# Kernel optimization log

Hardware: AMD Instinct MI355X
Metric: run time of the kernel (lower is better)

The kernel has to match this reference:

```python
import jax, jax.numpy as jnp
import numpy as np

NUM_EXPERTS = 8
D_MODEL = 2048
D_FF = 4096
TOP_K = 2
NUM_TOKENS = 4096


def setup_inputs() -> dict:
    key = jax.random.key(0)
    k1, k2, k3, k4, k5, k6 = jax.random.split(key, 6)
    hidden_states = jax.random.normal(k1, (NUM_TOKENS, D_MODEL), dtype=jnp.float32)
    top_k_index = jax.random.randint(k2, (NUM_TOKENS, TOP_K), 0, NUM_EXPERTS)
    raw = jax.random.uniform(k3, (NUM_TOKENS, TOP_K), dtype=jnp.float32)
    top_k_weights = raw / jnp.sum(raw, axis=-1, keepdims=True)  # normalized router weights
    scale = 0.02
    Wg = jax.random.normal(k4, (NUM_EXPERTS, D_MODEL, D_FF), dtype=jnp.float32) * scale
    Wu = jax.random.normal(k5, (NUM_EXPERTS, D_MODEL, D_FF), dtype=jnp.float32) * scale
    Wd = jax.random.normal(k6, (NUM_EXPERTS, D_FF, D_MODEL), dtype=jnp.float32) * scale
    return {
        "hidden_states": hidden_states,
        "top_k_index": top_k_index,
        "top_k_weights": top_k_weights,
        "Wg": Wg,
        "Wu": Wu,
        "Wd": Wd,
    }


def reference(hidden_states, top_k_index, top_k_weights, Wg, Wu, Wd):
    T, D = hidden_states.shape
    E = Wg.shape[0]
    # Combine weights: [T, E], summing duplicate expert hits exactly as the
    # original loop's repeated index_add_ would.
    combine = jnp.zeros((T, E), dtype=top_k_weights.dtype)
    combine = combine.at[jnp.arange(T)[:, None], top_k_index].add(top_k_weights)
    # Dense all-experts SwiGLU (same math per token/expert as the gather loop)
    gate = jnp.einsum("td,edf->tef", hidden_states, Wg)   # [T, E, F]
    up = jnp.einsum("td,edf->tef", hidden_states, Wu)     # [T, E, F]
    h = jax.nn.silu(gate) * up                              # [T, E, F]
    expert_out = jnp.einsum("tef,efd->ted", h, Wd)          # [T, E, D]
    # Weighted scatter-combine
    final = jnp.einsum("ted,te->td", expert_out, combine)   # [T, D]
    return final
```

## Files before the change

### kernel.cpp

```cpp
#include <hip/hip_runtime.h>
#include <hip/hip_bf16.h>

#define NTOK 4096
#define DM   2048
#define DF   4096
#define NEXP 8
#define NPAD 10240
#define NPTILE 40

typedef __attribute__((ext_vector_type(4))) float f32x4;
typedef __attribute__((ext_vector_type(8))) short s16x8;
typedef __attribute__((ext_vector_type(2))) int   i32x2;

__device__ __forceinline__ unsigned short f2bf(float f) {
  union { float f; unsigned u; } x; x.f = f;
  unsigned r = x.u + 0x7fffu + ((x.u >> 16) & 1u);
  return (unsigned short)(r >> 16);
}
__device__ __forceinline__ unsigned pack2(float lo, float hi) {
  __hip_bfloat162 h2 = __float22bfloat162_rn(make_float2(lo, hi));
  return *reinterpret_cast<unsigned*>(&h2);
}
__device__ __forceinline__ int swz(int row, int ks) {
  return row * 32 + ((ks ^ ((row >> 1) & 3)) << 3);
}
__device__ __forceinline__ void g2l16(const void* g, void* l) {
  __builtin_amdgcn_global_load_lds(
      (const __attribute__((address_space(1))) void*)g,
      (__attribute__((address_space(3))) void*)l, 16, 0, 0);
}

#define BARRIER() asm volatile("s_barrier" ::: "memory")
#define WAITV(n)  asm volatile("s_waitcnt vmcnt(" #n ")" ::: "memory")

__global__ void k_zero_out(float* out) {
  int gid = blockIdx.x * 256 + threadIdx.x;
  *(f32x4*)(out + (size_t)gid * 4) = f32x4{0.f, 0.f, 0.f, 0.f};
}

__global__ void k_init(int* tokrow, int* counts, int* cursor) {
  int i = blockIdx.x * 256 + threadIdx.x;
  if (i < NPAD) tokrow[i] = 0;
  if (i < NEXP) { counts[i] = 0; cursor[i] = 0; }
}

__global__ void k_count(const int* __restrict__ idx, int* counts) {
  int t = blockIdx.x * 256 + threadIdx.x;
  if (t >= NTOK) return;
  int e0 = idx[2 * t], e1 = idx[2 * t + 1];
  atomicAdd(&counts[e0], 1);
  if (e1 != e0) atomicAdd(&counts[e1], 1);
}

__global__ void k_scan(const int* __restrict__ counts, int* poff) {
  if (threadIdx.x == 0) {
    int s = 0;
    for (int e = 0; e < NEXP; e++) {
      poff[e] = s;
      s += ((counts[e] + 255) & ~255);
    }
  }
}

__global__ void k_fill(const int* __restrict__ idx, const float* __restrict__ wts,
                       const int* __restrict__ poff, int* cursor,
                       int* tokrow, float* wrow) {
  int t = blockIdx.x * 256 + threadIdx.x;
  if (t >= NTOK) return;
  int e0 = idx[2 * t], e1 = idx[2 * t + 1];
  float w0 = wts[2 * t], w1 = wts[2 * t + 1];
  if (e0 == e1) {
    int g = poff[e0] + atomicAdd(&cursor[e0], 1);
    tokrow[g] = t; wrow[g] = w0 + w1;
  } else {
    int g0 = poff[e0] + atomicAdd(&cursor[e0], 1);
    tokrow[g0] = t; wrow[g0] = w0;
    int g1 = poff[e1] + atomicAdd(&cursor[e1], 1);
    tokrow[g1] = t; wrow[g1] = w1;
  }
}

__global__ void k_convX(const float* __restrict__ X, const int* __restrict__ tokrow,
                        short* __restrict__ Xg) {
  const int kt = blockIdx.x, tile = blockIdx.y, tid = threadIdx.x;
  const int part = tid & 7;
  short* dst = Xg + (size_t)(tile * 64 + kt) * 8192;
  #pragma unroll
  for (int it = 0; it < 8; it++) {
    int row = it * 32 + (tid >> 3);
    int tok = tokrow[tile * 256 + row];
    f32x4 v = *(const f32x4*)(X + (size_t)tok * DM + kt * 32 + part * 4);
    i32x2 p;
    p[0] = (int)pack2(v[0], v[1]);
    p[1] = (int)pack2(v[2], v[3]);
    int idx = row * 32 + (((part >> 1) ^ ((row >> 1) & 3)) << 3) + (part & 1) * 4;
    *(i32x2*)&dst[idx] = p;
  }
}

__global__ void k_convW(const float* __restrict__ W, short* __restrict__ dst,
                        int N, int K) {
  const int nt = blockIdx.x, kt = blockIdx.y, e = blockIdx.z;
  const int t = threadIdx.x;
  const int kg = t >> 5, nb = t & 31;
  const float* src = W + (size_t)e * K * N + (size_t)(kt * 32 + kg * 4) * N
                     + nt * 128 + nb * 4;
  f32x4 b0 = *(const f32x4*)(src);
  f32x4 b1 = *(const f32x4*)(src + N);
  f32x4 b2 = *(const f32x4*)(src + 2 * (size_t)N);
  f32x4 b3 = *(const f32x4*)(src + 3 * (size_t)N);
  short* img = dst + ((size_t)(e * (N / 128) + nt) * (K / 32) + kt) * 4096;
  const int c0 = kg >> 1, klo = (kg & 1) * 4;
  #pragma unroll
  for (int j = 0; j < 4; j++) {
    int nl = nb * 4 + j;
    i32x2 v;
    v[0] = (int)pack2(b0[j], b1[j]);
    v[1] = (int)pack2(b2[j], b3[j]);
    *(i32x2*)&img[nl * 32 + ((c0 ^ ((nl >> 1) & 3)) << 3) + klo] = v;
  }
}

__global__ __launch_bounds__(512, 2) void gemm1_kernel(
    const short* __restrict__ Xg, const short* __restrict__ Wgt,
    const short* __restrict__ Wut, const int* __restrict__ counts,
    const int* __restrict__ poff, unsigned short* __restrict__ Hs) {
  const int e = blockIdx.z;
  const int cnt = counts[e];
  const int m0 = blockIdx.y * 256;
  if (m0 >= cnt) return;
  const int nt = blockIdx.x, n0 = nt * 128;
  const int tileIdx = (poff[e] >> 8) + blockIdx.y;

  __shared__ __attribute__((aligned(16))) short As[4][8192];
  __shared__ __attribute__((aligned(16))) short Bs[4][2][4096];

  const int tid = threadIdx.x, wave = tid >> 6, lane = tid & 63;
  const int wm = wave >> 1, wn = wave & 1;
  const int lr = lane & 15, ks = lane >> 4;

  const short* aSrc = Xg + (size_t)tileIdx * 64 * 8192 + wave * 1024 + lane * 8;
  const short* gSrc = Wgt + (size_t)(e * 32 + nt) * 64 * 4096 + wave * 512 + lane * 8;
  const short* uSrc = Wut + (size_t)(e * 32 + nt) * 64 * 4096 + wave * 512 + lane * 8;

  f32x4 accg[4][4], accu[4][4];
  #pragma unroll
  for (int i = 0; i < 4; i++)
    #pragma unroll
    for (int j = 0; j < 4; j++) {
      accg[i][j] = f32x4{0.f, 0.f, 0.f, 0.f};
      accu[i][j] = f32x4{0.f, 0.f, 0.f, 0.f};
    }

  auto stage = [&](int s, int kt) {
    g2l16(aSrc + (size_t)kt * 8192,       &As[s][wave * 1024]);
    g2l16(aSrc + (size_t)kt * 8192 + 512, &As[s][wave * 1024 + 512]);
    g2l16(gSrc + (size_t)kt * 4096,       &Bs[s][0][wave * 512]);
    g2l16(uSrc + (size_t)kt * 4096,       &Bs[s][1][wave * 512]);
  };

  const int nK = DM / 32;
  stage(0, 0); stage(1, 1); stage(2, 2);
  asm volatile("s_waitcnt vmcnt(8) lgkmcnt(0)" ::: "memory");
  BARRIER();

  for (int kt = 0; kt < nK; ++kt) {
    const int s = kt & 3;
    if (kt + 3 < nK) stage((kt + 3) & 3, kt + 3);
    s16x8 af[4], bg[4], bu[4];
    #pragma unroll
    for (int mi = 0; mi < 4; mi++)
      af[mi] = *(const s16x8*)&As[s][swz(wm * 64 + mi * 16 + lr, ks)];
    #pragma unroll
    for (int ni = 0; ni < 4; ni++) {
      bg[ni] = *(const s16x8*)&Bs[s][0][swz(wn * 64 + ni * 16 + lr, ks)];
      bu[ni] = *(const s16x8*)&Bs[s][1][swz(wn * 64 + ni * 16 + lr, ks)];
    }
    __builtin_amdgcn_s_setprio(1);
    #pragma unroll
    for (int mi = 0; mi < 4; mi++)
      #pragma unroll
      for (int ni = 0; ni < 4; ni++) {
        accg[mi][ni] = __builtin_amdgcn_mfma_f32_16x16x32_bf16(af[mi], bg[ni], accg[mi][ni], 0, 0, 0);
        accu[mi][ni] = __builtin_amdgcn_mfma_f32_16x16x32_bf16(af[mi], bu[ni], accu[mi][ni], 0, 0, 0);
      }
    __builtin_amdgcn_s_setprio(0);
    if (kt + 1 < nK) {
      if (kt + 3 < nK)      { WAITV(8); }
      else if (kt + 2 < nK) { WAITV(4); }
      else                  { WAITV(0); }
      BARRIER();
    }
  }

  const size_t tb = (size_t)tileIdx * 128 * 8192;
  #pragma unroll
  for (int mi = 0; mi < 4; mi++) {
    #pragma unroll
    for (int r = 0; r < 4; r++) {
      int row = wm * 64 + mi * 16 + ks * 4 + r;
      if (m0 + row < cnt) {
        #pragma unroll
        for (int ni = 0; ni < 4; ni++) {
          int col = n0 + wn * 64 + ni * 16 + lr;
          float g = accg[mi][ni][r], u = accu[mi][ni][r];
          float sv = g / (1.f + __expf(-g));
          int ktH = col >> 5, kl = col & 31;
          Hs[tb + (size_t)ktH * 8192 + row * 32 +
             (((kl >> 3) ^ ((row >> 1) & 3)) << 3) + (kl & 7)] = f2bf(sv * u);
        }
      }
    }
  }
}

__global__ __launch_bounds__(256, 2) void gemm2_kernel(
    const unsigned short* __restrict__ Hs, const short* __restrict__ Wdt,
    const int* __restrict__ counts, const int* __restrict__ poff,
    const int* __restrict__ tokrow, const float* __restrict__ wrow,
    float* __restrict__ out) {
  const int e = blockIdx.z;
  const int cnt = counts[e];
  const int m0 = blockIdx.y * 128;
  if (m0 >= cnt) return;
  const int nt = blockIdx.x, n0 = nt * 256;
  const int tileIdx = (poff[e] >> 8) + (m0 >> 8);
  const int half = (m0 >> 7) & 1;
  const int roff = poff[e];

  __shared__ __attribute__((aligned(16))) short As[3][4096];
  __shared__ __attribute__((aligned(16))) short Bs[3][2][4096];

  const int tid = threadIdx.x, wave = tid >> 6, lane = tid & 63;
  const int wm = wave >> 1, wn = wave & 1;
  const int lr = lane & 15, ks = lane >> 4;

  const unsigned short* aSrc = Hs + (size_t)tileIdx * 128 * 8192 + half * 4096
                               + wave * 1024 + lane * 8;
  const short* b0Src = Wdt + (size_t)(e * 16 + 2 * nt) * 128 * 4096
                       + wave * 1024 + lane * 8;
  const short* b1Src = Wdt + (size_t)(e * 16 + 2 * nt + 1) * 128 * 4096
                       + wave * 1024 + lane * 8;

  f32x4 acc0[4][4], acc1[4][4];
  #pragma unroll
  for (int i = 0; i < 4; i++)
    #pragma unroll
    for (int j = 0; j < 4; j++) {
      acc0[i][j] = f32x4{0.f, 0.f, 0.f, 0.f};
      acc1[i][j] = f32x4{0.f, 0.f, 0.f, 0.f};
    }

  auto stage = [&](int s, int kt) {
    g2l16(aSrc + (size_t)kt * 8192,        &As[s][wave * 1024]);
    g2l16(aSrc + (size_t)kt * 8192 + 512,  &As[s][wave * 1024 + 512]);
    g2l16(b0Src + (size_t)kt * 4096,       &Bs[s][0][wave * 1024]);
    g2l16(b0Src + (size_t)kt * 4096 + 512, &Bs[s][0][wave * 1024 + 512]);
    g2l16(b1Src + (size_t)kt * 4096,       &Bs[s][1][wave * 1024]);
    g2l16(b1Src + (size_t)kt * 4096 + 512, &Bs[s][1][wave * 1024 + 512]);
  };

  const int nK = DF / 32;
  stage(0, 0); stage(1, 1);
  WAITV(6);
  BARRIER();

  for (int kt = 0; kt < nK; ++kt) {
    const int s = kt % 3;
    if (kt + 2 < nK) stage((kt + 2) % 3, kt + 2);
    s16x8 af[4], b0f[4], b1f[4];
    #pragma unroll
    for (int mi = 0; mi < 4; mi++)
      af[mi] = *(const s16x8*)&As[s][swz(wm * 64 + mi * 16 + lr, ks)];
    #pragma unroll
    for (int ni = 0; ni < 4; ni++) {
      b0f[ni] = *(const s16x8*)&Bs[s][0][swz(wn * 64 + ni * 16 + lr, ks)];
      b1f[ni] = *(const s16x8*)&Bs[s][1][swz(wn * 64 + ni * 16 + lr, ks)];
    }
    __builtin_amdgcn_s_setprio(1);
    #pragma unroll
    for (int mi = 0; mi < 4; mi++)
      #pragma unroll
      for (int ni = 0; ni < 4; ni++) {
        acc0[mi][ni] = __builtin_amdgcn_mfma_f32_16x16x32_bf16(af[mi], b0f[ni], acc0[mi][ni], 0, 0, 0);
        acc1[mi][ni] = __builtin_amdgcn_mfma_f32_16x16x32_bf16(af[mi], b1f[ni], acc1[mi][ni], 0, 0, 0);
      }
    __builtin_amdgcn_s_setprio(0);
    if (kt + 1 < nK) {
      if (kt + 2 < nK) { WAITV(6); }
      else             { WAITV(0); }
      BARRIER();
    }
  }

  #pragma unroll
  for (int mi = 0; mi < 4; mi++) {
    #pragma unroll
    for (int r = 0; r < 4; r++) {
      int lrow = wm * 64 + mi * 16 + ks * 4 + r;
      if (m0 + lrow < cnt) {
        float wgt = wrow[roff + m0 + lrow];
        float* obase = out + (size_t)tokrow[roff + m0 + lrow] * DM + n0 + wn * 64 + lr;
        #pragma unroll
        for (int ni = 0; ni < 4; ni++) {
          atomicAdd(obase + ni * 16,       acc0[mi][ni][r] * wgt);
          atomicAdd(obase + 128 + ni * 16, acc1[mi][ni][r] * wgt);
        }
      }
    }
  }
}

extern "C" void kernel_launch(void* const* d_in, const int* in_sizes, int n_in,
                              void* d_out, int out_size, void* d_ws, size_t ws_size,
                              hipStream_t stream) {
  (void)in_sizes; (void)n_in; (void)out_size; (void)ws_size;
  const float* X   = (const float*)d_in[0];
  const int*   idx = (const int*)d_in[1];
  const float* wts = (const float*)d_in[2];
  const float* Wg  = (const float*)d_in[3];
  const float* Wu  = (const float*)d_in[4];
  const float* Wd  = (const float*)d_in[5];
  float* out = (float*)d_out;

  uint8_t* w = (uint8_t*)d_ws;
  int*   counts = (int*)(w + 0);
  int*   cursor = (int*)(w + 64);
  int*   poff   = (int*)(w + 128);
  int*   tokrow = (int*)(w + 4096);
  float* wrow   = (float*)(w + 49152);
  short* Xg     = (short*)(w + (1ull << 20));
  unsigned short* Hs = (unsigned short*)(w + (48ull << 20));
  short* Wgt    = (short*)(w + (128ull << 20));
  short* Wut    = (short*)(w + (256ull << 20));
  short* Wdt    = (short*)(w + (384ull << 20));

  k_zero_out<<<NTOK * DM / 1024, 256, 0, stream>>>(out);
  k_init<<<NPTILE, 256, 0, stream>>>(tokrow, counts, cursor);
  k_count<<<16, 256, 0, stream>>>(idx, counts);
  k_scan<<<1, 64, 0, stream>>>(counts, poff);
  k_fill<<<16, 256, 0, stream>>>(idx, wts, poff, cursor, tokrow, wrow);
  k_convX<<<dim3(DM / 32, NPTILE), 256, 0, stream>>>(X, tokrow, Xg);
  k_convW<<<dim3(DF / 128, DM / 32, NEXP), 256, 0, stream>>>(Wg, Wgt, DF, DM);
  k_convW<<<dim3(DF / 128, DM / 32, NEXP), 256, 0, stream>>>(Wu, Wut, DF, DM);
  k_convW<<<dim3(DM / 128, DF / 32, NEXP), 256, 0, stream>>>(Wd, Wdt, DM, DF);
  gemm1_kernel<<<dim3(DF / 128, 16, NEXP), 512, 0, stream>>>(Xg, Wgt, Wut, counts, poff, Hs);
  gemm2_kernel<<<dim3(DM / 256, 32, NEXP), 256, 0, stream>>>(Hs, Wdt, counts, poff, tokrow, wrow, out);
}
```

Measured before the change: 885.9 us.

## Overlap weight bf16 conversion with GEMM1 by co-scheduling blocks in one launch

Splits GEMM1 into two launches over experts 0-3 and 4-7. Each launch carries extra blocks that convert weights: the first converts gate/up weights for experts 4-7, the second converts all down-projection weights. Memory-bound conversion work can then overlap with compute-bound GEMM blocks instead of running as separate serial launches. The cost is a larger grid in which conversion blocks occupy GEMM-sized LDS slots, and correctness now depends on every GEMM block for a given expert reading only weights converted in an earlier launch.

Measured after the change: 899.3 us. About the same (+1.5%).

```diff
diff --git a/kernel.cpp b/kernel.cpp
--- a/kernel.cpp
+++ b/kernel.cpp
@@ -98,10 +98,9 @@
   }
 }
 
-__global__ void k_convW(const float* __restrict__ W, short* __restrict__ dst,
-                        int N, int K) {
-  const int nt = blockIdx.x, kt = blockIdx.y, e = blockIdx.z;
-  const int t = threadIdx.x;
+__device__ __forceinline__ void convW_image(
+    const float* __restrict__ W, short* __restrict__ dst,
+    int N, int K, int NT, int KT, int e, int nt, int kt, int t) {
   const int kg = t >> 5, nb = t & 31;
   const float* src = W + (size_t)e * K * N + (size_t)(kt * 32 + kg * 4) * N
                      + nt * 128 + nb * 4;
@@ -109,7 +108,7 @@
   f32x4 b1 = *(const f32x4*)(src + N);
   f32x4 b2 = *(const f32x4*)(src + 2 * (size_t)N);
   f32x4 b3 = *(const f32x4*)(src + 3 * (size_t)N);
-  short* img = dst + ((size_t)(e * (N / 128) + nt) * (K / 32) + kt) * 4096;
+  short* img = dst + ((size_t)(e * NT + nt) * KT + kt) * 4096;
   const int c0 = kg >> 1, klo = (kg & 1) * 4;
   #pragma unroll
   for (int j = 0; j < 4; j++) {
@@ -121,21 +120,51 @@
   }
 }
 
-__global__ __launch_bounds__(512, 2) void gemm1_kernel(
+__global__ void k_convW(const float* __restrict__ W, short* __restrict__ dst,
+                        int N, int K, int eBase) {
+  convW_image(W, dst, N, K, N / 128, K / 32, eBase + blockIdx.z,
+              blockIdx.x, blockIdx.y, threadIdx.x & 255);
+}
+
+__global__ __launch_bounds__(512, 2) void g1mix(
     const short* __restrict__ Xg, const short* __restrict__ Wgt,
     const short* __restrict__ Wut, const int* __restrict__ counts,
-    const int* __restrict__ poff, unsigned short* __restrict__ Hs) {
-  const int e = blockIdx.z;
-  const int cnt = counts[e];
-  const int m0 = blockIdx.y * 256;
-  if (m0 >= cnt) return;
-  const int nt = blockIdx.x, n0 = nt * 128;
-  const int tileIdx = (poff[e] >> 8) + blockIdx.y;
-
+    const int* __restrict__ poff, unsigned short* __restrict__ Hs, int e0g,
+    const float* __restrict__ srcA, short* __restrict__ dstA, int neA, int ebA,
+    const float* __restrict__ srcB, short* __restrict__ dstB, int neB, int ebB,
+    int Nc, int Kc) {
   __shared__ __attribute__((aligned(16))) short As[4][8192];
   __shared__ __attribute__((aligned(16))) short Bs[4][2][4096];
 
-  const int tid = threadIdx.x, wave = tid >> 6, lane = tid & 63;
+  const int bid = blockIdx.x;
+  const int tid = threadIdx.x;
+
+  if (bid >= 2048) {
+    (void)As; (void)Bs;
+    const int cu_ = bid - 2048;
+    const int perA = neA * 512;
+    const float* src; short* dst; int e;
+    if (cu_ < perA) { src = srcA; dst = dstA; e = ebA + (cu_ >> 9); }
+    else { const int r = cu_ - perA; src = srcB; dst = dstB; e = ebB + (r >> 9); }
+    const int unit = cu_ & 511;
+    const int NT = Nc / 128, KT = Kc / 32;
+    const int t = tid & 255;
+    #pragma unroll
+    for (int p = 0; p < 2; p++) {
+      int imgIdx = unit * 4 + p * 2 + (tid >> 8);
+      convW_image(src, dst, Nc, Kc, NT, KT, e, imgIdx / KT, imgIdx % KT, t);
+    }
+    return;
+  }
+
+  const int e = e0g + (bid >> 9);
+  const int cnt = counts[e];
+  const int m0 = ((bid >> 5) & 15) * 256;
+  if (m0 >= cnt) return;
+  const int nt = bid & 31, n0 = nt * 128;
+  const int tileIdx = (poff[e] >> 8) + ((bid >> 5) & 15);
+
+  const int wave = tid >> 6, lane = tid & 63;
   const int wm = wave >> 1, wn = wave & 1;
   const int lr = lane & 15, ks = lane >> 4;
 
@@ -341,9 +370,13 @@
   k_scan<<<1, 64, 0, stream>>>(counts, poff);
   k_fill<<<16, 256, 0, stream>>>(idx, wts, poff, cursor, tokrow, wrow);
   k_convX<<<dim3(DM / 32, NPTILE), 256, 0, stream>>>(X, tokrow, Xg);
-  k_convW<<<dim3(DF / 128, DM / 32, NEXP), 256, 0, stream>>>(Wg, Wgt, DF, DM);
-  k_convW<<<dim3(DF / 128, DM / 32, NEXP), 256, 0, stream>>>(Wu, Wut, DF, DM);
-  k_convW<<<dim3(DM / 128, DF / 32, NEXP), 256, 0, stream>>>(Wd, Wdt, DM, DF);
-  gemm1_kernel<<<dim3(DF / 128, 16, NEXP), 512, 0, stream>>>(Xg, Wgt, Wut, counts, poff, Hs);
+  k_convW<<<dim3(DF / 128, DM / 32, 4), 256, 0, stream>>>(Wg, Wgt, DF, DM, 0);
+  k_convW<<<dim3(DF / 128, DM / 32, 4), 256, 0, stream>>>(Wu, Wut, DF, DM, 0);
+  g1mix<<<2048 + 512 * 8, 512, 0, stream>>>(
+      Xg, Wgt, Wut, counts, poff, Hs, 0,
+      Wg, Wgt, 4, 4,  Wu, Wut, 4, 4,  DF, DM);
+  g1mix<<<2048 + 512 * 8, 512, 0, stream>>>(
+      Xg, Wgt, Wut, counts, poff, Hs, 4,
+      Wd, Wdt, 8, 0,  nullptr, nullptr, 0, 0,  DM, DF);
   gemm2_kernel<<<dim3(DM / 256, 32, NEXP), 256, 0, stream>>>(Hs, Wdt, counts, poff, tokrow, wrow, out);
 }
```
